# Kernel tuning notes

Measured on AMD Instinct MI355X. Metric: run time of the kernel, lower is better.

Reference implementation:

```python
import jax, jax.numpy as jnp
import numpy as np

N = 32768   # total nodes
E = 524288  # directed edges
F = 128     # input features
H = 128     # hidden width
G = 64      # graphs in batch (N//G = 512 nodes each)


def _lin(key, fan_in, fan_out):
    return jax.random.normal(key, (fan_in, fan_out), jnp.float32) / np.sqrt(fan_in)


def setup_inputs() -> dict:
    key = jax.random.key(0)
    ks = jax.random.split(key, 16)
    d = {}
    d["x"] = jax.random.normal(ks[0], (N, F), jnp.float32)
    d["edge_index"] = jax.random.randint(ks[1], (2, E), 0, N, dtype=jnp.int64)
    d["batch"] = (jnp.arange(N, dtype=jnp.int64) // (N // G))  # sorted, equal-size graphs
    # GCNConv 1 / 2
    d["W1"] = _lin(ks[2], F, H); d["b1"] = jnp.zeros((H,), jnp.float32)
    d["W2"] = _lin(ks[3], H, H); d["b2"] = jnp.zeros((H,), jnp.float32)
    # GraphSelfAttention (per-graph Q/K/V self-attention)
    d["Wq"] = _lin(ks[4], H, H); d["bq"] = jnp.zeros((H,), jnp.float32)
    d["Wk"] = _lin(ks[5], H, H); d["bk"] = jnp.zeros((H,), jnp.float32)
    d["Wv"] = _lin(ks[6], H, H); d["bv"] = jnp.zeros((H,), jnp.float32)
    # MLP head
    d["Wh1"] = _lin(ks[7], H, 64); d["bh1"] = jnp.zeros((64,), jnp.float32)
    d["Wh2"] = _lin(ks[8], 64, 1); d["bh2"] = jnp.zeros((1,), jnp.float32)
    return d


def gcn_conv(x, src, dst, W, b, num_nodes):
    """PyG-style GCNConv: D^{-1/2}(A+I)D^{-1/2} x W + b (self-loops already in src/dst)."""
    h = x @ W                                                    # [N, out]
    deg = jax.ops.segment_sum(jnp.ones_like(dst, dtype=h.dtype), dst,
                              num_segments=num_nodes)            # [N]
    dinv = jax.lax.rsqrt(jnp.maximum(deg, 1.0))
    norm = dinv[src] * dinv[dst]                                 # [E+N]
    msg = h[src] * norm[:, None]                                 # gather
    return jax.ops.segment_sum(msg, dst, num_segments=num_nodes) + b  # scatter-add


def reference(x, edge_index, batch, W1, b1, W2, b2, Wq, bq, Wk, bk, Wv, bv,
              Wh1, bh1, Wh2, bh2):
    num_nodes = x.shape[0]
    loop = jnp.arange(num_nodes, dtype=edge_index.dtype)
    src = jnp.concatenate([edge_index[0], loop])
    dst = jnp.concatenate([edge_index[1], loop])

    x = x.astype(jnp.float32)
    h = jax.nn.relu(gcn_conv(x, src, dst, W1, b1, num_nodes))    # dropout: eval mode (identity)
    h = jax.nn.relu(gcn_conv(h, src, dst, W2, b2, num_nodes))

    # batch = arange // n (equal-size sorted segments) -> dense reshape is exact
    n = num_nodes // G
    hg = h.reshape(G, n, H)                                      # [G, n, H]
    q = hg @ Wq + bq
    k = hg @ Wk + bk
    v = hg @ Wv + bv
    scores = jnp.einsum("gnd,gmd->gnm", q, k) / np.sqrt(H)       # [G, n, n]
    attn = jax.nn.softmax(scores, axis=-1)
    pooled = jnp.einsum("gnm,gmd->gnd", attn, v).mean(axis=1)    # [G, H]

    out = jax.nn.relu(pooled @ Wh1 + bh1) @ Wh2 + bh2            # [G, 1]
    return out
```

## Files before the change

### kernel.cpp

```cpp
#include <hip/hip_runtime.h>
#include <hip/hip_fp16.h>
#include <hip/hip_bf16.h>

#define NN 32768
#define GG 64
#define NPG 512
#define HD 128
#define MAXD 64
#define RSQRT_H 0.08838834764831845f

typedef _Float16 f16;
typedef __attribute__((ext_vector_type(4))) _Float16 f16x4;
typedef __attribute__((ext_vector_type(8))) _Float16 f16x8;
typedef __attribute__((ext_vector_type(4))) float f32x4;

__global__ void k_fill(const int* __restrict__ src, const int* __restrict__ dst,
                       int* __restrict__ cursor, int* __restrict__ ell, int E) {
    int e = blockIdx.x * 256 + threadIdx.x;
    if (e < E) {
        int d = dst[e];
        int slot = atomicAdd(&cursor[d], 1);
        if (slot < MAXD) ell[d * MAXD + slot] = src[e];
    }
}

__global__ void k_wprep(const float* __restrict__ W1, const float* __restrict__ W2,
                        const float* __restrict__ Wq, const float* __restrict__ Wk,
                        f16* __restrict__ wt) {
    const float* Ws[4] = {W1, W2, Wq, Wk};
    int k = blockIdx.x, wsel = blockIdx.y, n = threadIdx.x;
    float v = Ws[wsel][k * HD + n];
    wt[(size_t)wsel * HD * HD + n * HD + k] = (f16)v;
}

template<int AF32, int BIAS>
__global__ __launch_bounds__(256) void k_mgemm(
    const void* __restrict__ Ain, const f16* __restrict__ WT,
    const float* __restrict__ bias, f16* __restrict__ out)
{
    __shared__ f16 Al[64][136];
    __shared__ f16 Wl[128][136];
    int t = threadIdx.x;
    int row0 = blockIdx.x * 64;
    int w = t >> 6, lane = t & 63, lr = lane & 15, lu = lane >> 4;

    if (AF32) {
        const float4* A32 = (const float4*)((const float*)Ain + (size_t)row0 * HD);
#pragma unroll
        for (int i = 0; i < 8; ++i) {
            int idx = t + 256 * i;
            int r = idx >> 5, c4 = idx & 31;
            float4 v = A32[idx];
            f16x4 h = {(f16)v.x, (f16)v.y, (f16)v.z, (f16)v.w};
            *(f16x4*)&Al[r][c4 * 4] = h;
        }
    } else {
        const float4* A16 = (const float4*)((const f16*)Ain + (size_t)row0 * HD);
#pragma unroll
        for (int i = 0; i < 4; ++i) {
            int idx = t + 256 * i;
            int r = idx >> 4, cq = idx & 15;
            *(float4*)&Al[r][cq * 8] = A16[idx];
        }
    }
    const float4* W4 = (const float4*)WT;
#pragma unroll
    for (int i = 0; i < 8; ++i) {
        int idx = t + 256 * i;
        int n = idx >> 4, cq = idx & 15;
        *(float4*)&Wl[n][cq * 8] = W4[idx];
    }
    __syncthreads();

    f16x8 aq[4];
#pragma unroll
    for (int ks = 0; ks < 4; ++ks)
        aq[ks] = *(const f16x8*)&Al[w * 16 + lr][ks * 32 + lu * 8];

    f32x4 acc[8];
#pragma unroll
    for (int ni = 0; ni < 8; ++ni) {
        f32x4 c = {0.f, 0.f, 0.f, 0.f};
#pragma unroll
        for (int ks = 0; ks < 4; ++ks) {
            f16x8 b = *(const f16x8*)&Wl[ni * 16 + lr][ks * 32 + lu * 8];
            c = __builtin_amdgcn_mfma_f32_16x16x32_f16(aq[ks], b, c, 0, 0, 0);
        }
        acc[ni] = c;
    }

    __syncthreads();
#pragma unroll
    for (int ni = 0; ni < 8; ++ni)
#pragma unroll
        for (int j = 0; j < 4; ++j) {
            float v = acc[ni][j];
            if (BIAS) v += bias[ni * 16 + lr];
            Al[w * 16 + lu * 4 + j][ni * 16 + lr] = (f16)v;
        }
    __syncthreads();
    float4* O4 = (float4*)(out + (size_t)row0 * HD);
#pragma unroll
    for (int i = 0; i < 4; ++i) {
        int idx = t + 256 * i;
        int r = idx >> 4, cq = idx & 15;
        O4[idx] = *(float4*)&Al[r][cq * 8];
    }
}

__global__ __launch_bounds__(256) void k_agg(
    const __half* __restrict__ tmat, const int* __restrict__ cursor,
    const int* __restrict__ ell, const float* __restrict__ bias,
    __half* __restrict__ hout)
{
    int t = threadIdx.x;
    int i = blockIdx.x * 4 + (t >> 6);
    int lane = t & 63;
    int cnt = min(cursor[i], MAXD);
    float di = rsqrtf((float)(cnt + 1));
    float2 sv = __half22float2(((const __half2*)(tmat + (size_t)i * HD))[lane]);
    float acc0 = sv.x * (di * di);
    float acc1 = sv.y * (di * di);
    const int* row = ell + (size_t)i * MAXD;
    int e = 0;
    for (; e + 2 <= cnt; e += 2) {
        int s0 = row[e], s1 = row[e + 1];
        float w0 = rsqrtf((float)(min(cursor[s0], MAXD) + 1)) * di;
        float w1 = rsqrtf((float)(min(cursor[s1], MAXD) + 1)) * di;
        float2 v0 = __half22float2(((const __half2*)(tmat + (size_t)s0 * HD))[lane]);
        float2 v1 = __half22float2(((const __half2*)(tmat + (size_t)s1 * HD))[lane]);
        acc0 += v0.x * w0 + v1.x * w1;
        acc1 += v0.y * w0 + v1.y * w1;
    }
    if (e < cnt) {
        int s0 = row[e];
        float w0 = rsqrtf((float)(min(cursor[s0], MAXD) + 1)) * di;
        float2 v0 = __half22float2(((const __half2*)(tmat + (size_t)s0 * HD))[lane]);
        acc0 += v0.x * w0;
        acc1 += v0.y * w0;
    }
    int f = lane * 2;
    __half2 o;
    o.x = __float2half(fmaxf(acc0 + bias[f], 0.f));
    o.y = __float2half(fmaxf(acc1 + bias[f + 1], 0.f));
    ((__half2*)(hout + (size_t)i * HD))[lane] = o;
}

__global__ __launch_bounds__(256, 2) void k_attn(
    const __half* __restrict__ qh,
    const __half* __restrict__ kh,
    float* __restrict__ wpart)
{
    __shared__ f16 Kl[64][136];
    __shared__ float wlp[4][512];
    int t = threadIdx.x;
    int g = blockIdx.x >> 3;
    int qt = blockIdx.x & 7;
    int w = t >> 6, lane = t & 63;
    int lr = lane & 15, lu = lane >> 4;
    int qrow0 = g * NPG + qt * 64;

    f16x8 aq[4];
    {
        const f16* qp = (const f16*)qh + (size_t)(qrow0 + w * 16 + lr) * HD + lu * 8;
#pragma unroll
        for (int ks = 0; ks < 4; ++ks)
            aq[ks] = *(const f16x8*)(qp + ks * 32);
    }

    f32x4 p[8][4];
#pragma unroll
    for (int mt = 0; mt < 8; ++mt) {
        __syncthreads();
        {
            const float4* ks4 = (const float4*)(kh + (size_t)(g * NPG + mt * 64) * HD);
#pragma unroll
            for (int i = 0; i < 4; ++i) {
                int idx = t + 256 * i;
                int row = idx >> 4, cq = idx & 15;
                *(float4*)&Kl[row][cq * 8] = ks4[row * 16 + cq];
            }
        }
        __syncthreads();
#pragma unroll
        for (int ni = 0; ni < 4; ++ni) {
            f32x4 acc = {0.f, 0.f, 0.f, 0.f};
#pragma unroll
            for (int ks = 0; ks < 4; ++ks) {
                f16x8 b = *(const f16x8*)&Kl[ni * 16 + lr][ks * 32 + lu * 8];
                acc = __builtin_amdgcn_mfma_f32_16x16x32_f16(aq[ks], b, acc, 0, 0, 0);
            }
            p[mt][ni] = acc;
        }
    }

    float mrow[4], linv[4];
#pragma unroll
    for (int j = 0; j < 4; ++j) {
        float m = p[0][0][j];
#pragma unroll
        for (int mt = 0; mt < 8; ++mt)
#pragma unroll
            for (int ni = 0; ni < 4; ++ni) m = fmaxf(m, p[mt][ni][j]);
        m = fmaxf(m, __shfl_xor(m, 1));
        m = fmaxf(m, __shfl_xor(m, 2));
        m = fmaxf(m, __shfl_xor(m, 4));
        m = fmaxf(m, __shfl_xor(m, 8));
        mrow[j] = m;
    }
#pragma unroll
    for (int mt = 0; mt < 8; ++mt)
#pragma unroll
        for (int ni = 0; ni < 4; ++ni)
#pragma unroll
            for (int j = 0; j < 4; ++j)
                p[mt][ni][j] = __expf((p[mt][ni][j] - mrow[j]) * RSQRT_H);
#pragma unroll
    for (int j = 0; j < 4; ++j) {
        float l = 0.f;
#pragma unroll
        for (int mt = 0; mt < 8; ++mt)
#pragma unroll
            for (int ni = 0; ni < 4; ++ni) l += p[mt][ni][j];
        l += __shfl_xor(l, 1);
        l += __shfl_xor(l, 2);
        l += __shfl_xor(l, 4);
        l += __shfl_xor(l, 8);
        linv[j] = 1.f / l;
    }
#pragma unroll
    for (int mt = 0; mt < 8; ++mt)
#pragma unroll
        for (int ni = 0; ni < 4; ++ni) {
            float pc = p[mt][ni][0] * linv[0] + p[mt][ni][1] * linv[1]
                     + p[mt][ni][2] * linv[2] + p[mt][ni][3] * linv[3];
            pc += __shfl_xor(pc, 16);
            pc += __shfl_xor(pc, 32);
            if (lu == 0) wlp[w][mt * 64 + ni * 16 + lr] = pc;
        }
    __syncthreads();
    float* wp = wpart + ((size_t)(g * 8 + qt)) * NPG;
    wp[t] = (wlp[0][t] + wlp[1][t] + wlp[2][t] + wlp[3][t]) * (1.f / NPG);
    wp[t + 256] = (wlp[0][t + 256] + wlp[1][t + 256] + wlp[2][t + 256]
                 + wlp[3][t + 256]) * (1.f / NPG);
}

__global__ __launch_bounds__(128) void k_pool(
    const float* __restrict__ wpart, const __half* __restrict__ h,
    float* __restrict__ upart)
{
    __shared__ float wloc[64];
    int b = blockIdx.x;
    int g = b >> 3, ch = b & 7;
    int t = threadIdx.x;
    if (t < 64) {
        float w = 0.f;
#pragma unroll
        for (int qt = 0; qt < 8; ++qt)
            w += wpart[((size_t)(g * 8 + qt)) * NPG + ch * 64 + t];
        wloc[t] = w;
    }
    __syncthreads();
    const __half* hg = h + ((size_t)g * NPG + ch * 64) * HD;
    float u = 0.f;
#pragma unroll 4
    for (int m = 0; m < 64; ++m) u += wloc[m] * __half2float(hg[m * HD + t]);
    upart[(size_t)(ch * GG + g) * HD + t] = u;
}

__global__ __launch_bounds__(128) void k_head2(
    const float* __restrict__ upart,
    const float* __restrict__ Wv, const float* __restrict__ bv,
    const float* __restrict__ Wh1, const float* __restrict__ bh1,
    const float* __restrict__ Wh2, const float* __restrict__ bh2,
    float* __restrict__ out)
{
    __shared__ float ul[128];
    __shared__ float pl[128];
    __shared__ float r1l[64];
    int g = blockIdx.x, t = threadIdx.x;
    float ud = 0.f;
#pragma unroll
    for (int ch = 0; ch < 8; ++ch) ud += upart[(size_t)(ch * GG + g) * HD + t];
    ul[t] = ud;
    __syncthreads();
    float pv = bv[t];
    for (int d = 0; d < HD; ++d) pv += ul[d] * Wv[d * HD + t];
    pl[t] = pv;
    __syncthreads();
    if (t < 64) {
        float r1 = bh1[t];
        for (int d = 0; d < HD; ++d) r1 += pl[d] * Wh1[d * 64 + t];
        r1l[t] = fmaxf(r1, 0.f);
    }
    __syncthreads();
    if (t == 0) {
        float o = bh2[0];
        for (int j = 0; j < 64; ++j) o += r1l[j] * Wh2[j];
        out[g] = o;
    }
}

extern "C" void kernel_launch(void* const* d_in, const int* in_sizes, int n_in,
                              void* d_out, int out_size, void* d_ws, size_t ws_size,
                              hipStream_t stream) {
    const float* x   = (const float*)d_in[0];
    const int* edge  = (const int*)d_in[1];
    const float* W1  = (const float*)d_in[3];
    const float* b1  = (const float*)d_in[4];
    const float* W2  = (const float*)d_in[5];
    const float* b2  = (const float*)d_in[6];
    const float* Wq  = (const float*)d_in[7];
    const float* bq  = (const float*)d_in[8];
    const float* Wk  = (const float*)d_in[9];
    const float* bk  = (const float*)d_in[10];
    const float* Wv  = (const float*)d_in[11];
    const float* bv  = (const float*)d_in[12];
    const float* Wh1 = (const float*)d_in[13];
    const float* bh1 = (const float*)d_in[14];
    const float* Wh2 = (const float*)d_in[15];
    const float* bh2 = (const float*)d_in[16];
    float* out = (float*)d_out;

    int E = in_sizes[1] / 2;
    const int* src = edge;
    const int* dst = edge + E;

    float* tbuf = (float*)d_ws;
    float* hbr  = tbuf + (size_t)NN * HD;
    float* r3   = hbr + (size_t)NN * HD;
    float* wpart = r3 + (size_t)NN * HD;
    int* cursor = (int*)(wpart + GG * 8 * NPG);
    f16* wtb    = (f16*)(cursor + NN);
    __half* tmat = (__half*)tbuf;
    __half* qh   = (__half*)tbuf;
    __half* kh   = qh + (size_t)NN * HD;
    __half* hbuf = (__half*)hbr;
    int* ell    = (int*)r3;
    float* upart = r3;
    f16* W1T = wtb, *W2T = wtb + HD * HD, *WqT = wtb + 2 * HD * HD,
       * WkT = wtb + 3 * HD * HD;

    int eb = (E + 255) / 256;

    hipMemsetAsync(cursor, 0, NN * sizeof(int), stream);
    k_fill<<<eb, 256, 0, stream>>>(src, dst, cursor, ell, E);
    k_wprep<<<dim3(HD, 4), HD, 0, stream>>>(W1, W2, Wq, Wk, wtb);

    k_mgemm<1, 0><<<NN / 64, 256, 0, stream>>>(x, W1T, nullptr, (f16*)tmat);
    k_agg<<<NN / 4, 256, 0, stream>>>(tmat, cursor, ell, b1, hbuf);
    k_mgemm<0, 0><<<NN / 64, 256, 0, stream>>>(hbuf, W2T, nullptr, (f16*)tmat);
    k_agg<<<NN / 4, 256, 0, stream>>>(tmat, cursor, ell, b2, hbuf);
    k_mgemm<0, 1><<<NN / 64, 256, 0, stream>>>(hbuf, WqT, bq, (f16*)qh);
    k_mgemm<0, 1><<<NN / 64, 256, 0, stream>>>(hbuf, WkT, bk, (f16*)kh);
    k_attn<<<GG * 8, 256, 0, stream>>>(qh, kh, wpart);
    k_pool<<<GG * 8, 128, 0, stream>>>(wpart, hbuf, upart);
    k_head2<<<GG, 128, 0, stream>>>(upart, Wv, bv, Wh1, bh1, Wh2, bh2, out);
}
```

Measured before the change: 262.1 us.

## Fuse GCN aggregation with following GEMMs, double-buffer K tiles, merge pool and head

Aggregation is now fused into the following GEMM kernels. conv1 aggregation runs with the W2 GEMM, and conv2 aggregation runs with both the Q and K projections. The aggregated tile stays in shared memory, so the intermediate h no longer round-trips through global memory. The attention kernel double-buffers K tiles to remove one barrier per tile, and the pool and head kernels are merged into one launch. The trade-off is that the fused kernels have only 512 blocks doing gather-heavy aggregation with 16 rows per wave, which reduces parallelism compared with the previous 8192-block aggregation.

```diff
diff --git a/kernel.cpp b/kernel.cpp
--- a/kernel.cpp
+++ b/kernel.cpp
@@ -33,10 +33,9 @@
     wt[(size_t)wsel * HD * HD + n * HD + k] = (f16)v;
 }
 
-template<int AF32, int BIAS>
-__global__ __launch_bounds__(256) void k_mgemm(
-    const void* __restrict__ Ain, const f16* __restrict__ WT,
-    const float* __restrict__ bias, f16* __restrict__ out)
+__global__ __launch_bounds__(256) void k_mgemm1(
+    const float* __restrict__ Ain, const f16* __restrict__ WT,
+    f16* __restrict__ out)
 {
     __shared__ f16 Al[64][136];
     __shared__ f16 Wl[128][136];
@@ -44,31 +43,20 @@
     int row0 = blockIdx.x * 64;
     int w = t >> 6, lane = t & 63, lr = lane & 15, lu = lane >> 4;
 
-    if (AF32) {
-        const float4* A32 = (const float4*)((const float*)Ain + (size_t)row0 * HD);
-#pragma unroll
-        for (int i = 0; i < 8; ++i) {
-            int idx = t + 256 * i;
-            int r = idx >> 5, c4 = idx & 31;
-            float4 v = A32[idx];
-            f16x4 h = {(f16)v.x, (f16)v.y, (f16)v.z, (f16)v.w};
-            *(f16x4*)&Al[r][c4 * 4] = h;
-        }
-    } else {
-        const float4* A16 = (const float4*)((const f16*)Ain + (size_t)row0 * HD);
-#pragma unroll
-        for (int i = 0; i < 4; ++i) {
-            int idx = t + 256 * i;
-            int r = idx >> 4, cq = idx & 15;
-            *(float4*)&Al[r][cq * 8] = A16[idx];
-        }
-    }
     const float4* W4 = (const float4*)WT;
 #pragma unroll
     for (int i = 0; i < 8; ++i) {
         int idx = t + 256 * i;
-        int n = idx >> 4, cq = idx & 15;
-        *(float4*)&Wl[n][cq * 8] = W4[idx];
+        *(float4*)&Wl[idx >> 4][(idx & 15) * 8] = W4[idx];
+    }
+    const float4* A32 = (const float4*)(Ain + (size_t)row0 * HD);
+#pragma unroll
+    for (int i = 0; i < 8; ++i) {
+        int idx = t + 256 * i;
+        int r = idx >> 5, c4 = idx & 31;
+        float4 v = A32[idx];
+        f16x4 h = {(f16)v.x, (f16)v.y, (f16)v.z, (f16)v.w};
+        *(f16x4*)&Al[r][c4 * 4] = h;
     }
     __syncthreads();
 
@@ -76,7 +64,6 @@
 #pragma unroll
     for (int ks = 0; ks < 4; ++ks)
         aq[ks] = *(const f16x8*)&Al[w * 16 + lr][ks * 32 + lu * 8];
-
     f32x4 acc[8];
 #pragma unroll
     for (int ni = 0; ni < 8; ++ni) {
@@ -88,62 +75,200 @@
         }
         acc[ni] = c;
     }
-
     __syncthreads();
 #pragma unroll
     for (int ni = 0; ni < 8; ++ni)
 #pragma unroll
-        for (int j = 0; j < 4; ++j) {
-            float v = acc[ni][j];
-            if (BIAS) v += bias[ni * 16 + lr];
-            Al[w * 16 + lu * 4 + j][ni * 16 + lr] = (f16)v;
-        }
+        for (int j = 0; j < 4; ++j)
+            Al[w * 16 + lu * 4 + j][ni * 16 + lr] = (f16)acc[ni][j];
     __syncthreads();
     float4* O4 = (float4*)(out + (size_t)row0 * HD);
 #pragma unroll
     for (int i = 0; i < 4; ++i) {
         int idx = t + 256 * i;
-        int r = idx >> 4, cq = idx & 15;
-        O4[idx] = *(float4*)&Al[r][cq * 8];
-    }
-}
-
-__global__ __launch_bounds__(256) void k_agg(
+        O4[idx] = *(float4*)&Al[idx >> 4][(idx & 15) * 8];
+    }
+}
+
+__device__ __forceinline__ void agg_rows(
     const __half* __restrict__ tmat, const int* __restrict__ cursor,
     const int* __restrict__ ell, const float* __restrict__ bias,
-    __half* __restrict__ hout)
-{
+    int row0, int w, int lane, f16 (*Al)[136], __half* __restrict__ hout)
+{
+    int lane2 = lane * 2;
+    float b0 = bias[lane2], b1 = bias[lane2 + 1];
+    for (int n = 0; n < 16; ++n) {
+        int i = row0 + w * 16 + n;
+        int cnt = min(cursor[i], MAXD);
+        float di = rsqrtf((float)(cnt + 1));
+        float2 sv = __half22float2(((const __half2*)(tmat + (size_t)i * HD))[lane]);
+        float a0 = sv.x * (di * di), a1 = sv.y * (di * di);
+        const int* row = ell + (size_t)i * MAXD;
+        int e = 0;
+        for (; e + 4 <= cnt; e += 4) {
+            int s0 = row[e], s1 = row[e + 1], s2 = row[e + 2], s3 = row[e + 3];
+            float q0 = rsqrtf((float)(min(cursor[s0], MAXD) + 1)) * di;
+            float q1 = rsqrtf((float)(min(cursor[s1], MAXD) + 1)) * di;
+            float q2 = rsqrtf((float)(min(cursor[s2], MAXD) + 1)) * di;
+            float q3 = rsqrtf((float)(min(cursor[s3], MAXD) + 1)) * di;
+            float2 v0 = __half22float2(((const __half2*)(tmat + (size_t)s0 * HD))[lane]);
+            float2 v1 = __half22float2(((const __half2*)(tmat + (size_t)s1 * HD))[lane]);
+            float2 v2 = __half22float2(((const __half2*)(tmat + (size_t)s2 * HD))[lane]);
+            float2 v3 = __half22float2(((const __half2*)(tmat + (size_t)s3 * HD))[lane]);
+            a0 += v0.x * q0 + v1.x * q1 + v2.x * q2 + v3.x * q3;
+            a1 += v0.y * q0 + v1.y * q1 + v2.y * q2 + v3.y * q3;
+        }
+        for (; e < cnt; ++e) {
+            int s0 = row[e];
+            float q0 = rsqrtf((float)(min(cursor[s0], MAXD) + 1)) * di;
+            float2 v0 = __half22float2(((const __half2*)(tmat + (size_t)s0 * HD))[lane]);
+            a0 += v0.x * q0;
+            a1 += v0.y * q0;
+        }
+        a0 = fmaxf(a0 + b0, 0.f);
+        a1 = fmaxf(a1 + b1, 0.f);
+        __half2 o;
+        o.x = __float2half(a0); o.y = __float2half(a1);
+        *(__half2*)&Al[w * 16 + n][lane2] = *(__half2*)&o;
+        if (hout) ((__half2*)(hout + (size_t)i * HD))[lane] = o;
+    }
+}
+
+__global__ __launch_bounds__(256) void k_convA(
+    const __half* __restrict__ t1, const int* __restrict__ cursor,
+    const int* __restrict__ ell, const float* __restrict__ b1,
+    const f16* __restrict__ W2T, f16* __restrict__ t2)
+{
+    __shared__ f16 Al[64][136];
+    __shared__ f16 Wl[128][136];
     int t = threadIdx.x;
-    int i = blockIdx.x * 4 + (t >> 6);
-    int lane = t & 63;
-    int cnt = min(cursor[i], MAXD);
-    float di = rsqrtf((float)(cnt + 1));
-    float2 sv = __half22float2(((const __half2*)(tmat + (size_t)i * HD))[lane]);
-    float acc0 = sv.x * (di * di);
-    float acc1 = sv.y * (di * di);
-    const int* row = ell + (size_t)i * MAXD;
-    int e = 0;
-    for (; e + 2 <= cnt; e += 2) {
-        int s0 = row[e], s1 = row[e + 1];
-        float w0 = rsqrtf((float)(min(cursor[s0], MAXD) + 1)) * di;
-        float w1 = rsqrtf((float)(min(cursor[s1], MAXD) + 1)) * di;
-        float2 v0 = __half22float2(((const __half2*)(tmat + (size_t)s0 * HD))[lane]);
-        float2 v1 = __half22float2(((const __half2*)(tmat + (size_t)s1 * HD))[lane]);
-        acc0 += v0.x * w0 + v1.x * w1;
-        acc1 += v0.y * w0 + v1.y * w1;
-    }
-    if (e < cnt) {
-        int s0 = row[e];
-        float w0 = rsqrtf((float)(min(cursor[s0], MAXD) + 1)) * di;
-        float2 v0 = __half22float2(((const __half2*)(tmat + (size_t)s0 * HD))[lane]);
-        acc0 += v0.x * w0;
-        acc1 += v0.y * w0;
-    }
-    int f = lane * 2;
-    __half2 o;
-    o.x = __float2half(fmaxf(acc0 + bias[f], 0.f));
-    o.y = __float2half(fmaxf(acc1 + bias[f + 1], 0.f));
-    ((__half2*)(hout + (size_t)i * HD))[lane] = o;
+    int row0 = blockIdx.x * 64;
+    int w = t >> 6, lane = t & 63, lr = lane & 15, lu = lane >> 4;
+
+    const float4* W4 = (const float4*)W2T;
+#pragma unroll
+    for (int i = 0; i < 8; ++i) {
+        int idx = t + 256 * i;
+        *(float4*)&Wl[idx >> 4][(idx & 15) * 8] = W4[idx];
+    }
+    agg_rows(t1, cursor, ell, b1, row0, w, lane, Al, nullptr);
+    __syncthreads();
+
+    f16x8 aq[4];
+#pragma unroll
+    for (int ks = 0; ks < 4; ++ks)
+        aq[ks] = *(const f16x8*)&Al[w * 16 + lr][ks * 32 + lu * 8];
+    f32x4 acc[8];
+#pragma unroll
+    for (int ni = 0; ni < 8; ++ni) {
+        f32x4 c = {0.f, 0.f, 0.f, 0.f};
+#pragma unroll
+        for (int ks = 0; ks < 4; ++ks) {
+            f16x8 b = *(const f16x8*)&Wl[ni * 16 + lr][ks * 32 + lu * 8];
+            c = __builtin_amdgcn_mfma_f32_16x16x32_f16(aq[ks], b, c, 0, 0, 0);
+        }
+        acc[ni] = c;
+    }
+    __syncthreads();
+#pragma unroll
+    for (int ni = 0; ni < 8; ++ni)
+#pragma unroll
+        for (int j = 0; j < 4; ++j)
+            Al[w * 16 + lu * 4 + j][ni * 16 + lr] = (f16)acc[ni][j];
+    __syncthreads();
+    float4* O4 = (float4*)(t2 + (size_t)row0 * HD);
+#pragma unroll
+    for (int i = 0; i < 4; ++i) {
+        int idx = t + 256 * i;
+        O4[idx] = *(float4*)&Al[idx >> 4][(idx & 15) * 8];
+    }
+}
+
+__global__ __launch_bounds__(256) void k_convB(
+    const __half* __restrict__ t2, const int* __restrict__ cursor,
+    const int* __restrict__ ell, const float* __restrict__ b2,
+    const f16* __restrict__ WqT, const float* __restrict__ bq,
+    const f16* __restrict__ WkT, const float* __restrict__ bk,
+    __half* __restrict__ hout, f16* __restrict__ qout, f16* __restrict__ kout)
+{
+    __shared__ f16 Al[64][136];
+    __shared__ f16 Wl[128][136];
+    int t = threadIdx.x;
+    int row0 = blockIdx.x * 64;
+    int w = t >> 6, lane = t & 63, lr = lane & 15, lu = lane >> 4;
+
+    const float4* Wq4 = (const float4*)WqT;
+#pragma unroll
+    for (int i = 0; i < 8; ++i) {
+        int idx = t + 256 * i;
+        *(float4*)&Wl[idx >> 4][(idx & 15) * 8] = Wq4[idx];
+    }
+    agg_rows(t2, cursor, ell, b2, row0, w, lane, Al, hout);
+    __syncthreads();
+
+    f16x8 aq[4];
+#pragma unroll
+    for (int ks = 0; ks < 4; ++ks)
+        aq[ks] = *(const f16x8*)&Al[w * 16 + lr][ks * 32 + lu * 8];
+    f32x4 acc[8];
+#pragma unroll
+    for (int ni = 0; ni < 8; ++ni) {
+        f32x4 c = {0.f, 0.f, 0.f, 0.f};
+#pragma unroll
+        for (int ks = 0; ks < 4; ++ks) {
+            f16x8 b = *(const f16x8*)&Wl[ni * 16 + lr][ks * 32 + lu * 8];
+            c = __builtin_amdgcn_mfma_f32_16x16x32_f16(aq[ks], b, c, 0, 0, 0);
+        }
+        acc[ni] = c;
+    }
+    __syncthreads();
+    const float4* Wk4 = (const float4*)WkT;
+#pragma unroll
+    for (int i = 0; i < 8; ++i) {
+        int idx = t + 256 * i;
+        *(float4*)&Wl[idx >> 4][(idx & 15) * 8] = Wk4[idx];
+    }
+#pragma unroll
+    for (int ni = 0; ni < 8; ++ni)
+#pragma unroll
+        for (int j = 0; j < 4; ++j)
+            Al[w * 16 + lu * 4 + j][ni * 16 + lr] =
+                (f16)(acc[ni][j] + bq[ni * 16 + lr]);
+    __syncthreads();
+    {
+        float4* O4 = (float4*)(qout + (size_t)row0 * HD);
+#pragma unroll
+        for (int i = 0; i < 4; ++i) {
+            int idx = t + 256 * i;
+            O4[idx] = *(float4*)&Al[idx >> 4][(idx & 15) * 8];
+        }
+    }
+#pragma unroll
+    for (int ni = 0; ni < 8; ++ni) {
+        f32x4 c = {0.f, 0.f, 0.f, 0.f};
+#pragma unroll
+        for (int ks = 0; ks < 4; ++ks) {
+            f16x8 b = *(const f16x8*)&Wl[ni * 16 + lr][ks * 32 + lu * 8];
+            c = __builtin_amdgcn_mfma_f32_16x16x32_f16(aq[ks], b, c, 0, 0, 0);
+        }
+        acc[ni] = c;
+    }
+    __syncthreads();
+#pragma unroll
+    for (int ni = 0; ni < 8; ++ni)
+#pragma unroll
+        for (int j = 0; j < 4; ++j)
+            Al[w * 16 + lu * 4 + j][ni * 16 + lr] =
+                (f16)(acc[ni][j] + bk[ni * 16 + lr]);
+    __syncthreads();
+    {
+        float4* O4 = (float4*)(kout + (size_t)row0 * HD);
+#pragma unroll
+        for (int i = 0; i < 4; ++i) {
+            int idx = t + 256 * i;
+            O4[idx] = *(float4*)&Al[idx >> 4][(idx & 15) * 8];
+        }
+    }
 }
 
 __global__ __launch_bounds__(256, 2) void k_attn(
@@ -151,7 +276,7 @@
     const __half* __restrict__ kh,
     float* __restrict__ wpart)
 {
-    __shared__ f16 Kl[64][136];
+    __shared__ f16 Kl[2][64][136];
     __shared__ float wlp[4][512];
     int t = threadIdx.x;
     int g = blockIdx.x >> 3;
@@ -167,27 +292,33 @@
         for (int ks = 0; ks < 4; ++ks)
             aq[ks] = *(const f16x8*)(qp + ks * 32);
     }
+    {
+        const float4* ks4 = (const float4*)(kh + (size_t)(g * NPG) * HD);
+#pragma unroll
+        for (int i = 0; i < 4; ++i) {
+            int idx = t + 256 * i;
+            *(float4*)&Kl[0][idx >> 4][(idx & 15) * 8] = ks4[idx];
+        }
+    }
 
     f32x4 p[8][4];
 #pragma unroll
     for (int mt = 0; mt < 8; ++mt) {
         __syncthreads();
-        {
-            const float4* ks4 = (const float4*)(kh + (size_t)(g * NPG + mt * 64) * HD);
+        if (mt < 7) {
+            const float4* ks4 = (const float4*)(kh + (size_t)(g * NPG + (mt + 1) * 64) * HD);
 #pragma unroll
             for (int i = 0; i < 4; ++i) {
                 int idx = t + 256 * i;
-                int row = idx >> 4, cq = idx & 15;
-                *(float4*)&Kl[row][cq * 8] = ks4[row * 16 + cq];
+                *(float4*)&Kl[(mt + 1) & 1][idx >> 4][(idx & 15) * 8] = ks4[idx];
             }
         }
-        __syncthreads();
 #pragma unroll
         for (int ni = 0; ni < 4; ++ni) {
             f32x4 acc = {0.f, 0.f, 0.f, 0.f};
 #pragma unroll
             for (int ks = 0; ks < 4; ++ks) {
-                f16x8 b = *(const f16x8*)&Kl[ni * 16 + lr][ks * 32 + lu * 8];
+                f16x8 b = *(const f16x8*)&Kl[mt & 1][ni * 16 + lr][ks * 32 + lu * 8];
                 acc = __builtin_amdgcn_mfma_f32_16x16x32_f16(aq[ks], b, acc, 0, 0, 0);
             }
             p[mt][ni] = acc;
@@ -245,48 +376,44 @@
                  + wlp[3][t + 256]) * (1.f / NPG);
 }
 
-__global__ __launch_bounds__(128) void k_pool(
+__global__ __launch_bounds__(256) void k_poolhead(
     const float* __restrict__ wpart, const __half* __restrict__ h,
-    float* __restrict__ upart)
-{
-    __shared__ float wloc[64];
-    int b = blockIdx.x;
-    int g = b >> 3, ch = b & 7;
-    int t = threadIdx.x;
-    if (t < 64) {
-        float w = 0.f;
-#pragma unroll
-        for (int qt = 0; qt < 8; ++qt)
-            w += wpart[((size_t)(g * 8 + qt)) * NPG + ch * 64 + t];
-        wloc[t] = w;
-    }
-    __syncthreads();
-    const __half* hg = h + ((size_t)g * NPG + ch * 64) * HD;
-    float u = 0.f;
-#pragma unroll 4
-    for (int m = 0; m < 64; ++m) u += wloc[m] * __half2float(hg[m * HD + t]);
-    upart[(size_t)(ch * GG + g) * HD + t] = u;
-}
-
-__global__ __launch_bounds__(128) void k_head2(
-    const float* __restrict__ upart,
     const float* __restrict__ Wv, const float* __restrict__ bv,
     const float* __restrict__ Wh1, const float* __restrict__ bh1,
     const float* __restrict__ Wh2, const float* __restrict__ bh2,
     float* __restrict__ out)
 {
+    __shared__ float wloc[512];
+    __shared__ float upar[2][128];
     __shared__ float ul[128];
     __shared__ float pl[128];
     __shared__ float r1l[64];
     int g = blockIdx.x, t = threadIdx.x;
-    float ud = 0.f;
-#pragma unroll
-    for (int ch = 0; ch < 8; ++ch) ud += upart[(size_t)(ch * GG + g) * HD + t];
-    ul[t] = ud;
-    __syncthreads();
-    float pv = bv[t];
-    for (int d = 0; d < HD; ++d) pv += ul[d] * Wv[d * HD + t];
-    pl[t] = pv;
+    {
+        float w0 = 0.f, w1 = 0.f;
+#pragma unroll
+        for (int qt = 0; qt < 8; ++qt) {
+            const float* wp = wpart + ((size_t)(g * 8 + qt)) * NPG;
+            w0 += wp[t]; w1 += wp[t + 256];
+        }
+        wloc[t] = w0; wloc[t + 256] = w1;
+    }
+    __syncthreads();
+    int col = t & 127, half = t >> 7;
+    const __half* hg = h + ((size_t)g * NPG + half * 256) * HD;
+    float u = 0.f;
+#pragma unroll 4
+    for (int m = 0; m < 256; ++m)
+        u += wloc[half * 256 + m] * __half2float(hg[(size_t)m * HD + col]);
+    upar[half][col] = u;
+    __syncthreads();
+    if (t < 128) ul[t] = upar[0][t] + upar[1][t];
+    __syncthreads();
+    if (t < 128) {
+        float pv = bv[t];
+        for (int d = 0; d < HD; ++d) pv += ul[d] * Wv[d * HD + t];
+        pl[t] = pv;
+    }
     __syncthreads();
     if (t < 64) {
         float r1 = bh1[t];
@@ -326,18 +453,15 @@
     const int* src = edge;
     const int* dst = edge + E;
 
-    float* tbuf = (float*)d_ws;
-    float* hbr  = tbuf + (size_t)NN * HD;
-    float* r3   = hbr + (size_t)NN * HD;
-    float* wpart = r3 + (size_t)NN * HD;
+    f16* t1 = (f16*)d_ws;
+    f16* t2 = t1 + (size_t)NN * HD;
+    __half* h2 = (__half*)(t2 + (size_t)NN * HD);
+    f16* qh = (f16*)(h2 + (size_t)NN * HD);
+    int* ell = (int*)(qh + (size_t)NN * HD);
+    f16* kh = (f16*)(ell + (size_t)NN * MAXD);
+    float* wpart = (float*)(kh + (size_t)NN * HD);
     int* cursor = (int*)(wpart + GG * 8 * NPG);
     f16* wtb    = (f16*)(cursor + NN);
-    __half* tmat = (__half*)tbuf;
-    __half* qh   = (__half*)tbuf;
-    __half* kh   = qh + (size_t)NN * HD;
-    __half* hbuf = (__half*)hbr;
-    int* ell    = (int*)r3;
-    float* upart = r3;
     f16* W1T = wtb, *W2T = wtb + HD * HD, *WqT = wtb + 2 * HD * HD,
        * WkT = wtb + 3 * HD * HD;
 
@@ -347,13 +471,10 @@
     k_fill<<<eb, 256, 0, stream>>>(src, dst, cursor, ell, E);
     k_wprep<<<dim3(HD, 4), HD, 0, stream>>>(W1, W2, Wq, Wk, wtb);
 
-    k_mgemm<1, 0><<<NN / 64, 256, 0, stream>>>(x, W1T, nullptr, (f16*)tmat);
-    k_agg<<<NN / 4, 256, 0, stream>>>(tmat, cursor, ell, b1, hbuf);
-    k_mgemm<0, 0><<<NN / 64, 256, 0, stream>>>(hbuf, W2T, nullptr, (f16*)tmat);
-    k_agg<<<NN / 4, 256, 0, stream>>>(tmat, cursor, ell, b2, hbuf);
-    k_mgemm<0, 1><<<NN / 64, 256, 0, stream>>>(hbuf, WqT, bq, (f16*)qh);
-    k_mgemm<0, 1><<<NN / 64, 256, 0, stream>>>(hbuf, WkT, bk, (f16*)kh);
-    k_attn<<<GG * 8, 256, 0, stream>>>(qh, kh, wpart);
-    k_pool<<<GG * 8, 128, 0, stream>>>(wpart, hbuf, upart);
-    k_head2<<<GG, 128, 0, stream>>>(upart, Wv, bv, Wh1, bh1, Wh2, bh2, out);
-}
+    k_mgemm1<<<NN / 64, 256, 0, stream>>>(x, W1T, t1);
+    k_convA<<<NN / 64, 256, 0, stream>>>((const __half*)t1, cursor, ell, b1, W2T, t2);
+    k_convB<<<NN / 64, 256, 0, stream>>>((const __half*)t2, cursor, ell, b2,
+                                         WqT, bq, WkT, bk, h2, qh, kh);
+    k_attn<<<GG * 8, 256, 0, stream>>>((const __half*)qh, (const __half*)kh, wpart);
+    k_poolhead<<<GG, 256, 0, stream>>>(wpart, h2, Wv, bv, Wh1, bh1, Wh2, bh2, out);
+}
```

Measured after the change: 309.6 us. 1.18x slower.
